# Kernel tuning notes

Hardware: AMD Instinct MI355X
Metric: run time of the kernel (lower is better)

The kernel has to match this reference:

```python
import jax, jax.numpy as jnp
import numpy as np

E = 8      # num_traits / experts
D = 1024   # input_size per trait
H = 2048   # hidden width (hidden_sizes = [2048, 2048] -> one hidden Linear)
O = 1024   # output_size
B = 4096   # batch
TOP_K = 2


def setup_inputs() -> dict:
    key = jax.random.key(0)
    ks = jax.random.split(key, E + 8)
    s = 0.02
    inp = {f"x{i}": jax.random.normal(ks[i], (B, D), dtype=jnp.float32) for i in range(E)}
    inp["gate_w"] = jax.random.normal(ks[E + 0], (E * D, E), dtype=jnp.float32) * s
    inp["gate_b"] = jnp.zeros((E,), dtype=jnp.float32)
    inp["w_in"]  = jax.random.normal(ks[E + 1], (E, D, H), dtype=jnp.float32) * s
    inp["b_in"]  = jnp.zeros((E, H), dtype=jnp.float32)
    inp["w_h"]   = jax.random.normal(ks[E + 2], (E, H, H), dtype=jnp.float32) * s
    inp["b_h"]   = jnp.zeros((E, H), dtype=jnp.float32)
    inp["w_out"] = jax.random.normal(ks[E + 3], (E, H, O), dtype=jnp.float32) * s
    inp["b_out"] = jnp.zeros((E, O), dtype=jnp.float32)
    return inp


def reference(x0, x1, x2, x3, x4, x5, x6, x7,
              gate_w, gate_b, w_in, b_in, w_h, b_h, w_out, b_out):
    xs_list = [x0, x1, x2, x3, x4, x5, x6, x7]
    xs = jnp.stack(xs_list, axis=0)                       # [E, B, D]
    combined = jnp.concatenate(xs_list, axis=1)           # [B, E*D]

    # gating: top-2 + softmax over selected logits, scattered to dense [B, E]
    gate_logits = combined @ gate_w + gate_b              # [B, E]
    topk_vals, topk_idx = jax.lax.top_k(gate_logits, TOP_K)
    topk_w = jax.nn.softmax(topk_vals, axis=1)
    bsz = gate_logits.shape[0]
    rows = jnp.arange(bsz)[:, None]
    dense_w = jnp.zeros_like(gate_logits).at[rows, topk_idx].set(topk_w)  # [B, E]

    # per-expert MLP (dropout inactive at inference; use_skip=False).
    # Computed densely for all tokens; unselected tokens get weight 0 in the
    # combine, matching the masked dispatch/scatter math exactly.
    h = jax.nn.relu(jnp.einsum('ebd,edh->ebh', xs, w_in) + b_in[:, None, :])   # [E, B, H]
    h = jax.nn.relu(jnp.einsum('ebh,ehk->ebk', h, w_h) + b_h[:, None, :])      # [E, B, H]
    expert_out = jnp.einsum('ebk,eko->ebo', h, w_out) + b_out[:, None, :]      # [E, B, O]

    # weighted combine: sum_e dense_w[b,e] * expert_out[e,b,:]
    moe_output = jnp.einsum('ebo,be->bo', expert_out, dense_w)                 # [B, O]
    return moe_output
```

## Files before the change

kernel.cpp:

```cpp
#include <hip/hip_runtime.h>
#include <stdint.h>

#define E_ 8
#define D_ 1024
#define H_ 2048
#define O_ 1024
#define B_ 4096
#define GTOT (B_ * 2)
#define GPAD (GTOT + 256)
#define MT_MAX 16
#define MT256 8

typedef __attribute__((ext_vector_type(8))) __bf16 bf16x8;
typedef __attribute__((ext_vector_type(4))) float f32x4;
typedef unsigned short u16;
typedef __attribute__((ext_vector_type(4))) u16 u16x4;
typedef __attribute__((ext_vector_type(8))) u16 u16x8;

__device__ __forceinline__ u16 f2bf(float f) {
    union { float f; uint32_t u; } v; v.f = f;
    uint32_t u = v.u;
    return (u16)((u + 0x7FFFu + ((u >> 16) & 1u)) >> 16);
}

__device__ __forceinline__ void gl2lds16(const void* g, void* lds) {
    __builtin_amdgcn_global_load_lds(
        (__attribute__((address_space(1))) void*)(uintptr_t)g,
        (__attribute__((address_space(3))) void*)(uint32_t)(uintptr_t)lds,
        16, 0, 0);
}

struct XPtrs { const float* p[8]; };

__device__ __forceinline__ void gate_finish(int b, const double* acc, const float* __restrict__ gb,
                                            int* __restrict__ t2i, float* __restrict__ t2w) {
    float lg[8];
#pragma unroll
    for (int e = 0; e < 8; ++e) lg[e] = (float)acc[e] + gb[e];
    int i0 = 0;
#pragma unroll
    for (int e = 1; e < 8; ++e) if (lg[e] > lg[i0]) i0 = e;
    int i1 = -1;
#pragma unroll
    for (int e = 0; e < 8; ++e) {
        if (e == i0) continue;
        if (i1 < 0 || lg[e] > lg[i1]) i1 = e;
    }
    float ex = expf(lg[i1] - lg[i0]);
    float w0 = 1.0f / (1.0f + ex);
    t2i[b * 2 + 0] = i0; t2i[b * 2 + 1] = i1;
    t2w[b * 2 + 0] = w0; t2w[b * 2 + 1] = ex * w0;
}

__global__ void __launch_bounds__(256) gate_kernel(XPtrs xs, const float* __restrict__ gw,
                                                   const float* __restrict__ gb,
                                                   int* __restrict__ t2i, float* __restrict__ t2w) {
    int wave = threadIdx.x >> 6;
    int lane = threadIdx.x & 63;
    int b0 = blockIdx.x * 8 + wave * 2;
    double acc0[8], acc1[8];
#pragma unroll
    for (int e = 0; e < 8; ++e) { acc0[e] = 0.0; acc1[e] = 0.0; }
    for (int ep = 0; ep < 8; ++ep) {
        const float* xr0 = xs.p[ep] + (size_t)b0 * D_;
        const float* xr1 = xr0 + D_;
        for (int t = 0; t < D_ / 64; ++t) {
            int d = t * 64 + lane;
            float v0 = xr0[d];
            float v1 = xr1[d];
            const float* g = gw + ((size_t)(ep * D_ + d)) * 8;
#pragma unroll
            for (int e = 0; e < 8; ++e) {
                double ge = (double)g[e];
                acc0[e] += (double)v0 * ge;
                acc1[e] += (double)v1 * ge;
            }
        }
    }
#pragma unroll
    for (int e = 0; e < 8; ++e) {
        for (int off = 32; off > 0; off >>= 1) {
            acc0[e] += __shfl_xor(acc0[e], off, 64);
            acc1[e] += __shfl_xor(acc1[e], off, 64);
        }
    }
    if (lane == 0) {
        gate_finish(b0 + 0, acc0, gb, t2i, t2w);
        gate_finish(b0 + 1, acc1, gb, t2i, t2w);
    }
}

__global__ void __launch_bounds__(256) route_build(const int* __restrict__ t2i,
                                                   int* __restrict__ offs, int* __restrict__ cursor) {
    __shared__ int cnt[8];
    int t = threadIdx.x;
    if (t < 8) cnt[t] = 0;
    __syncthreads();
    for (int i = t; i < B_ * 2; i += 256) atomicAdd(&cnt[t2i[i]], 1);
    __syncthreads();
    if (t == 0) {
        int run = 0;
        for (int e = 0; e < 8; ++e) { offs[e] = run; cursor[e] = run; run += cnt[e]; }
        offs[8] = run;
    }
}

__global__ void __launch_bounds__(256) scatter_gather(XPtrs xs, const int* __restrict__ t2i,
                                                      int* __restrict__ cursor, int* __restrict__ slot,
                                                      u16* __restrict__ A1) {
    int b = blockIdx.x;
    int t = threadIdx.x;
    __shared__ int gsh[2];
    int e0 = t2i[b * 2 + 0], e1 = t2i[b * 2 + 1];
    if (t == 0) {
        int g0 = atomicAdd(&cursor[e0], 1);
        int g1 = atomicAdd(&cursor[e1], 1);
        gsh[0] = g0; gsh[1] = g1;
        slot[b * 2 + 0] = g0; slot[b * 2 + 1] = g1;
    }
    __syncthreads();
    int g0 = gsh[0], g1 = gsh[1];
    float4 v0 = ((const float4*)(xs.p[e0] + (size_t)b * D_))[t];
    float4 v1 = ((const float4*)(xs.p[e1] + (size_t)b * D_))[t];
    u16x4 o0, o1;
    o0.x = f2bf(v0.x); o0.y = f2bf(v0.y); o0.z = f2bf(v0.z); o0.w = f2bf(v0.w);
    o1.x = f2bf(v1.x); o1.y = f2bf(v1.y); o1.z = f2bf(v1.z); o1.w = f2bf(v1.w);
    ((u16x4*)(A1 + (size_t)g0 * D_))[t] = o0;
    ((u16x4*)(A1 + (size_t)g1 * D_))[t] = o1;
}

__global__ void __launch_bounds__(256) wconv(const float* __restrict__ w, u16* __restrict__ wt,
                                             int K, int N) {
    __shared__ float tile[64][33];
    int e = blockIdx.z;
    int n0 = blockIdx.x * 32, k0 = blockIdx.y * 64;
    int tid = threadIdx.x;
    int tx = tid & 31, ty = tid >> 5;
    const float* wp = w + (size_t)e * K * N + (size_t)k0 * N + n0;
#pragma unroll
    for (int r = 0; r < 8; ++r)
        tile[ty + r * 8][tx] = wp[(size_t)(ty + r * 8) * N + tx];
    __syncthreads();
    int n = tid >> 3, kq = tid & 7;
    u16x8 o;
#pragma unroll
    for (int i = 0; i < 8; ++i) o[i] = f2bf(tile[kq * 8 + i][n]);
    u16* op = wt + (size_t)e * N * K + (size_t)(n0 + n) * K + k0 + kq * 8;
    *(u16x8*)op = o;
}

__global__ void __launch_bounds__(512, 2) expert_gemm256(const u16* __restrict__ A,
                                                         const u16* __restrict__ Wt,
                                                         const float* __restrict__ bias,
                                                         u16* __restrict__ outB,
                                                         const int* __restrict__ offs,
                                                         int K, int N) {
    int bid = blockIdx.x;
    int e = bid & 7;
    int j = bid >> 3;
    int mt = j & (MT256 - 1);
    int nt = j >> 3;
    int row0 = offs[e];
    int cnt = offs[e + 1] - row0;
    if (mt * 256 >= cnt) return;

    extern __shared__ __align__(16) u16 smem[];
    u16* sA = smem;
    u16* sB = smem + 32768;

    int tid = threadIdx.x;
    int wave = tid >> 6, lane = tid & 63;
    int wm = wave >> 2;
    int wn = wave & 3;
    int l15 = lane & 15, quad = lane >> 4;
    int swz = l15 & 7;

    const u16* Abase = A + (size_t)(row0 + mt * 256) * K;
    const u16* Bbase = Wt + ((size_t)e * N + (size_t)nt * 256) * K;
    int NT = K >> 6;

    auto stageA = [&](int tile, int half) {
        if (tile < NT) {
            u16* dst = sA + (((tile & 1) * 2 + half) << 13);
            const u16* gs = Abase + (size_t)(half * 128) * K + tile * 64;
#pragma unroll
            for (int rr = 0; rr < 2; ++rr) {
                int liB = rr * 512 + wave * 64;
                int li = liB + lane;
                int r = li >> 3;
                int lc = (li & 7) ^ (r & 7);
                gl2lds16(gs + (size_t)r * K + lc * 8, dst + liB * 8);
            }
        }
    };
    auto stageB = [&](int tile, int half) {
        if (tile < NT) {
            u16* dst = sB + (((tile & 1) * 2 + half) << 13);
            const u16* gs = Bbase + (size_t)(half * 128) * K + tile * 64;
#pragma unroll
            for (int rr = 0; rr < 2; ++rr) {
                int liB = rr * 512 + wave * 64;
                int li = liB + lane;
                int r = li >> 3;
                int lc = (li & 7) ^ (r & 7);
                gl2lds16(gs + (size_t)r * K + lc * 8, dst + liB * 8);
            }
        }
    };

    f32x4 acc[2][2][4][2];
#pragma unroll
    for (int a = 0; a < 2; ++a)
#pragma unroll
        for (int b = 0; b < 2; ++b)
#pragma unroll
            for (int c = 0; c < 4; ++c)
#pragma unroll
                for (int dd = 0; dd < 2; ++dd) acc[a][b][c][dd] = (f32x4){0.f, 0.f, 0.f, 0.f};

    stageA(0, 0); stageB(0, 0); stageA(0, 1); stageB(0, 1);
    stageA(1, 0); stageB(1, 0);
    __builtin_amdgcn_s_waitcnt(0x74);
    __builtin_amdgcn_s_barrier();

    bf16x8 af[4][2];
    bf16x8 bfr[2][2][2];

    for (int T = 0; T < NT; ++T) {
        int d = T & 1;
        const u16* aB0 = sA + ((d * 2 + 0) << 13);
        const u16* aB1 = sA + ((d * 2 + 1) << 13);
        const u16* bB0 = sB + ((d * 2 + 0) << 13);
        const u16* bB1 = sB + ((d * 2 + 1) << 13);

#pragma unroll
        for (int fm = 0; fm < 4; ++fm) {
            int rh = wm * 64 + fm * 16 + l15;
#pragma unroll
            for (int kc = 0; kc < 2; ++kc)
                af[fm][kc] = *(const bf16x8*)(aB0 + rh * 64 + (((kc << 2) | quad) ^ swz) * 8);
        }
#pragma unroll
        for (int fn = 0; fn < 2; ++fn) {
            int rh = wn * 32 + fn * 16 + l15;
#pragma unroll
            for (int kc = 0; kc < 2; ++kc)
                bfr[0][fn][kc] = *(const bf16x8*)(bB0 + rh * 64 + (((kc << 2) | quad) ^ swz) * 8);
        }
        stageA(T + 1, 1);
        __builtin_amdgcn_s_barrier();
        __builtin_amdgcn_s_setprio(1);
#pragma unroll
        for (int fm = 0; fm < 4; ++fm)
#pragma unroll
            for (int fn = 0; fn < 2; ++fn)
#pragma unroll
                for (int kc = 0; kc < 2; ++kc)
                    acc[0][0][fm][fn] = __builtin_amdgcn_mfma_f32_16x16x32_bf16(
                        af[fm][kc], bfr[0][fn][kc], acc[0][0][fm][fn], 0, 0, 0);
        __builtin_amdgcn_s_setprio(0);
        __builtin_amdgcn_s_barrier();

#pragma unroll
        for (int fn = 0; fn < 2; ++fn) {
            int rh = wn * 32 + fn * 16 + l15;
#pragma unroll
            for (int kc = 0; kc < 2; ++kc)
                bfr[1][fn][kc] = *(const bf16x8*)(bB1 + rh * 64 + (((kc << 2) | quad) ^ swz) * 8);
        }
        stageB(T + 1, 1);
        __builtin_amdgcn_s_barrier();
        __builtin_amdgcn_s_setprio(1);
#pragma unroll
        for (int fm = 0; fm < 4; ++fm)
#pragma unroll
            for (int fn = 0; fn < 2; ++fn)
#pragma unroll
                for (int kc = 0; kc < 2; ++kc)
                    acc[0][1][fm][fn] = __builtin_amdgcn_mfma_f32_16x16x32_bf16(
                        af[fm][kc], bfr[1][fn][kc], acc[0][1][fm][fn], 0, 0, 0);
        __builtin_amdgcn_s_setprio(0);
        __builtin_amdgcn_s_barrier();

#pragma unroll
        for (int fm = 0; fm < 4; ++fm) {
            int rh = wm * 64 + fm * 16 + l15;
#pragma unroll
            for (int kc = 0; kc < 2; ++kc)
                af[fm][kc] = *(const bf16x8*)(aB1 + rh * 64 + (((kc << 2) | quad) ^ swz) * 8);
        }
        stageA(T + 2, 0);
        __builtin_amdgcn_s_barrier();
        __builtin_amdgcn_s_setprio(1);
#pragma unroll
        for (int fm = 0; fm < 4; ++fm)
#pragma unroll
            for (int fn = 0; fn < 2; ++fn)
#pragma unroll
                for (int kc = 0; kc < 2; ++kc)
                    acc[1][0][fm][fn] = __builtin_amdgcn_mfma_f32_16x16x32_bf16(
                        af[fm][kc], bfr[0][fn][kc], acc[1][0][fm][fn], 0, 0, 0);
        __builtin_amdgcn_s_setprio(0);
        __builtin_amdgcn_s_barrier();

        stageB(T + 2, 0);
        __builtin_amdgcn_s_barrier();
        __builtin_amdgcn_s_setprio(1);
#pragma unroll
        for (int fm = 0; fm < 4; ++fm)
#pragma unroll
            for (int fn = 0; fn < 2; ++fn)
#pragma unroll
                for (int kc = 0; kc < 2; ++kc)
                    acc[1][1][fm][fn] = __builtin_amdgcn_mfma_f32_16x16x32_bf16(
                        af[fm][kc], bfr[1][fn][kc], acc[1][1][fm][fn], 0, 0, 0);
        __builtin_amdgcn_s_setprio(0);
        if (T + 2 < NT) __builtin_amdgcn_s_waitcnt(0x74);
        else            __builtin_amdgcn_s_waitcnt(0x70);
        __builtin_amdgcn_s_barrier();
    }

#pragma unroll
    for (int mh = 0; mh < 2; ++mh)
#pragma unroll
        for (int nh = 0; nh < 2; ++nh)
#pragma unroll
            for (int fn = 0; fn < 2; ++fn) {
                int col = nt * 256 + nh * 128 + wn * 32 + fn * 16 + l15;
                float bv = bias[e * N + col];
#pragma unroll
                for (int fm = 0; fm < 4; ++fm) {
                    int rloc = mt * 256 + mh * 128 + wm * 64 + fm * 16 + quad * 4;
#pragma unroll
                    for (int r = 0; r < 4; ++r) {
                        if (rloc + r < cnt) {
                            float v = acc[mh][nh][fm][fn][r] + bv;
                            v = fmaxf(v, 0.f);
                            outB[(size_t)(row0 + rloc + r) * N + col] = f2bf(v);
                        }
                    }
                }
            }
}

__global__ void __launch_bounds__(256) expert_gemm(const u16* __restrict__ A, const u16* __restrict__ Wt,
                                                   const float* __restrict__ bias,
                                                   u16* __restrict__ outB, float* __restrict__ outF,
                                                   const int* __restrict__ offs, int K, int N, int relu) {
    int bid = blockIdx.x;
    int e = bid & 7;
    int j = bid >> 3;
    int mt = j & (MT_MAX - 1);
    int nt = j >> 4;
    int row0 = offs[e];
    int cnt = offs[e + 1] - row0;
    if (mt * 128 >= cnt) return;

    __shared__ __align__(16) u16 sA[3][128 * 32];
    __shared__ __align__(16) u16 sB[3][128 * 32];

    int tid = threadIdx.x;
    int wave = tid >> 6, lane = tid & 63;
    int wm = wave & 1, wn = wave >> 1;
    int l15 = lane & 15, quad = lane >> 4;
    int rsub = lane >> 2;
    int koff = (((lane & 3) ^ (rsub & 3) ^ ((rsub >> 2) & 3)) * 8);
    int physOff = (quad ^ (l15 & 3) ^ ((l15 >> 2) & 3)) * 8;

    f32x4 acc[4][4];
#pragma unroll
    for (int i = 0; i < 4; ++i)
#pragma unroll
        for (int jj = 0; jj < 4; ++jj) acc[i][jj] = (f32x4){0.f, 0.f, 0.f, 0.f};

    const u16* Abase = A + (size_t)(row0 + mt * 128) * K;
    const u16* Bbase = Wt + ((size_t)e * N + (size_t)nt * 128) * K;

    int kSteps = K / 32;

    auto issue = [&](int ks, int bufIdx) {
        int k0 = ks * 32;
        u16* dA = &sA[bufIdx][0];
        u16* dB = &sB[bufIdx][0];
#pragma unroll
        for (int c = 0; c < 2; ++c) {
            int ch = wave * 2 + c;
            int r = ch * 16 + rsub;
            gl2lds16(Abase + (size_t)r * K + k0 + koff, dA + ch * 512);
            gl2lds16(Bbase + (size_t)r * K + k0 + koff, dB + ch * 512);
        }
    };

    issue(0, 0);
    issue(1, 1);
    int bc = 0, bi = 2;
    for (int ks = 0; ks < kSteps; ++ks) {
        if (ks + 1 < kSteps) __builtin_amdgcn_s_waitcnt(0x74);
        else                 __builtin_amdgcn_s_waitcnt(0x70);
        __builtin_amdgcn_s_barrier();
        if (ks + 2 < kSteps) issue(ks + 2, bi);

        const u16* a_ = &sA[bc][0];
        const u16* b_ = &sB[bc][0];
        bf16x8 af[4], bfr[4];
#pragma unroll
        for (int tm = 0; tm < 4; ++tm) {
            int row = wm * 64 + tm * 16 + l15;
            af[tm] = *(const bf16x8*)(a_ + row * 32 + physOff);
        }
#pragma unroll
        for (int tn = 0; tn < 4; ++tn) {
            int row = wn * 64 + tn * 16 + l15;
            bfr[tn] = *(const bf16x8*)(b_ + row * 32 + physOff);
        }
        __builtin_amdgcn_s_setprio(1);
#pragma unroll
        for (int tm = 0; tm < 4; ++tm)
#pragma unroll
            for (int tn = 0; tn < 4; ++tn)
                acc[tm][tn] = __builtin_amdgcn_mfma_f32_16x16x32_bf16(af[tm], bfr[tn], acc[tm][tn], 0, 0, 0);
        __builtin_amdgcn_s_setprio(0);

        bc = (bc == 2) ? 0 : bc + 1;
        bi = (bi == 2) ? 0 : bi + 1;
    }

    size_t gm0 = (size_t)row0 + (size_t)mt * 128 + (size_t)wm * 64;
    int lm0 = mt * 128 + wm * 64;
    int n0 = nt * 128 + wn * 64;
#pragma unroll
    for (int tn = 0; tn < 4; ++tn) {
        int col = n0 + tn * 16 + l15;
        float bv = bias[e * N + col];
#pragma unroll
        for (int tm = 0; tm < 4; ++tm) {
#pragma unroll
            for (int r = 0; r < 4; ++r) {
                int rr = tm * 16 + quad * 4 + r;
                if (lm0 + rr < cnt) {
                    float v = acc[tm][tn][r] + bv;
                    if (relu) v = fmaxf(v, 0.f);
                    if (outB) outB[(gm0 + rr) * N + col] = f2bf(v);
                    else      outF[(gm0 + rr) * N + col] = v;
                }
            }
        }
    }
}

__global__ void __launch_bounds__(256) combine_out(const float* __restrict__ eo, const int* __restrict__ slot,
                                                   const float* __restrict__ t2w, float* __restrict__ out) {
    int b = blockIdx.x, t = threadIdx.x;
    int g0 = slot[b * 2 + 0], g1 = slot[b * 2 + 1];
    float w0 = t2w[b * 2 + 0], w1 = t2w[b * 2 + 1];
    float4 va = ((const float4*)(eo + (size_t)g0 * O_))[t];
    float4 vc = ((const float4*)(eo + (size_t)g1 * O_))[t];
    float4 r;
    r.x = w0 * va.x + w1 * vc.x;
    r.y = w0 * va.y + w1 * vc.y;
    r.z = w0 * va.z + w1 * vc.z;
    r.w = w0 * va.w + w1 * vc.w;
    ((float4*)(out + (size_t)b * O_))[t] = r;
}

extern "C" void kernel_launch(void* const* d_in, const int* in_sizes, int n_in,
                              void* d_out, int out_size, void* d_ws, size_t ws_size,
                              hipStream_t stream) {
    (void)in_sizes; (void)n_in; (void)out_size; (void)ws_size;

    static bool lds_attr_set = false;
    if (!lds_attr_set) {
        hipFuncSetAttribute((const void*)expert_gemm256,
                            hipFuncAttributeMaxDynamicSharedMemorySize, 131072);
        lds_attr_set = true;
    }

    XPtrs xp;
    for (int i = 0; i < 8; ++i) xp.p[i] = (const float*)d_in[i];
    const float* gate_w = (const float*)d_in[8];
    const float* gate_b = (const float*)d_in[9];
    const float* w_in  = (const float*)d_in[10];
    const float* b_in  = (const float*)d_in[11];
    const float* w_h   = (const float*)d_in[12];
    const float* b_h   = (const float*)d_in[13];
    const float* w_out = (const float*)d_in[14];
    const float* b_out = (const float*)d_in[15];
    float* out = (float*)d_out;

    char* ws = (char*)d_ws;
    size_t off = 0;
    auto alloc = [&](size_t b) { size_t o = off; off += (b + 255) & ~(size_t)255; return o; };

    size_t t2i_o  = alloc((size_t)B_ * 2 * 4);
    size_t t2w_o  = alloc((size_t)B_ * 2 * 4);
    size_t slot_o = alloc((size_t)B_ * 2 * 4);
    size_t offs_o = alloc(16 * 4);
    size_t cur_o  = alloc(8 * 4);
    size_t A1_o   = alloc((size_t)GPAD * D_ * 2);
    size_t h1_o   = alloc((size_t)GPAD * H_ * 2);
    size_t h2_o   = alloc((size_t)GPAD * H_ * 2);
    size_t wtin_o = alloc((size_t)E_ * H_ * D_ * 2);
    size_t wth_o  = alloc((size_t)E_ * H_ * H_ * 2);
    size_t wtout_o= alloc((size_t)E_ * O_ * H_ * 2);
    size_t eo_o   = A1_o;

    int*   t2i  = (int*)(ws + t2i_o);
    float* t2w  = (float*)(ws + t2w_o);
    int*   slot = (int*)(ws + slot_o);
    int*   offs = (int*)(ws + offs_o);
    int*   cur  = (int*)(ws + cur_o);
    u16*   A1   = (u16*)(ws + A1_o);
    u16*   h1   = (u16*)(ws + h1_o);
    u16*   h2   = (u16*)(ws + h2_o);
    u16*   wtin = (u16*)(ws + wtin_o);
    u16*   wth  = (u16*)(ws + wth_o);
    u16*   wtout= (u16*)(ws + wtout_o);
    float* eo   = (float*)(ws + eo_o);

    hipLaunchKernelGGL(gate_kernel, dim3(B_ / 8), dim3(256), 0, stream, xp, gate_w, gate_b, t2i, t2w);
    hipLaunchKernelGGL(route_build, dim3(1), dim3(256), 0, stream, t2i, offs, cur);
    hipLaunchKernelGGL(scatter_gather, dim3(B_), dim3(256), 0, stream, xp, t2i, cur, slot, A1);

    hipLaunchKernelGGL(wconv, dim3(H_ / 32, D_ / 64, E_), dim3(256), 0, stream, w_in, wtin, D_, H_);
    hipLaunchKernelGGL(wconv, dim3(H_ / 32, H_ / 64, E_), dim3(256), 0, stream, w_h, wth, H_, H_);
    hipLaunchKernelGGL(wconv, dim3(O_ / 32, H_ / 64, E_), dim3(256), 0, stream, w_out, wtout, H_, O_);

    hipLaunchKernelGGL(expert_gemm256, dim3(E_ * MT256 * (H_ / 256)), dim3(512), 131072, stream,
                       A1, wtin, b_in, h1, offs, D_, H_);
    hipLaunchKernelGGL(expert_gemm256, dim3(E_ * MT256 * (H_ / 256)), dim3(512), 131072, stream,
                       h1, wth, b_h, h2, offs, H_, H_);
    hipLaunchKernelGGL(expert_gemm, dim3(E_ * MT_MAX * (O_ / 128)), dim3(256), 0, stream,
                       h2, wtout, b_out, (u16*)nullptr, eo, offs, H_, O_, 0);

    hipLaunchKernelGGL(combine_out, dim3(B_), dim3(256), 0, stream, eo, slot, t2w, out);
}
```

Before: 838.9 us.

## Double-buffer LDS fragment registers to overlap reads with MFMA in GEMM loop

Reorganizes the main GEMM k-loop so LDS-to-register fragment reads for the next quadrant (and next tile) are issued before the current MFMA block runs. It uses separate A and B register buffers and adjusts the waitcnt values to match. The goal is to hide LDS read latency behind matrix instructions and remove stalls at quadrant boundaries. In exchange it raises VGPR pressure, which could hurt occupancy, and it depends on finely tuned waitcnt encodings being correct.

```diff
diff --git a/kernel.cpp b/kernel.cpp
--- a/kernel.cpp
+++ b/kernel.cpp
@@ -208,6 +208,40 @@
         }
     };
 
+    bf16x8 afA[4][2], afB[4][2];
+    bf16x8 bf0[2][2], bf1[2][2];
+
+    auto readA = [&](bf16x8 (&dst)[4][2], const u16* base) {
+#pragma unroll
+        for (int fm = 0; fm < 4; ++fm) {
+            int rh = wm * 64 + fm * 16 + l15;
+#pragma unroll
+            for (int kc = 0; kc < 2; ++kc)
+                dst[fm][kc] = *(const bf16x8*)(base + rh * 64 + (((kc << 2) | quad) ^ swz) * 8);
+        }
+    };
+    auto readB = [&](bf16x8 (&dst)[2][2], const u16* base) {
+#pragma unroll
+        for (int fn = 0; fn < 2; ++fn) {
+            int rh = wn * 32 + fn * 16 + l15;
+#pragma unroll
+            for (int kc = 0; kc < 2; ++kc)
+                dst[fn][kc] = *(const bf16x8*)(base + rh * 64 + (((kc << 2) | quad) ^ swz) * 8);
+        }
+    };
+    auto mfmaQ = [&](bf16x8 (&a)[4][2], bf16x8 (&b)[2][2], f32x4 (&ac)[4][2]) {
+        __builtin_amdgcn_s_setprio(1);
+#pragma unroll
+        for (int fm = 0; fm < 4; ++fm)
+#pragma unroll
+            for (int fn = 0; fn < 2; ++fn)
+#pragma unroll
+                for (int kc = 0; kc < 2; ++kc)
+                    ac[fm][fn] = __builtin_amdgcn_mfma_f32_16x16x32_bf16(
+                        a[fm][kc], b[fn][kc], ac[fm][fn], 0, 0, 0);
+        __builtin_amdgcn_s_setprio(0);
+    };
+
     f32x4 acc[2][2][4][2];
 #pragma unroll
     for (int a = 0; a < 2; ++a)
@@ -220,105 +254,52 @@
 
     stageA(0, 0); stageB(0, 0); stageA(0, 1); stageB(0, 1);
     stageA(1, 0); stageB(1, 0);
-    __builtin_amdgcn_s_waitcnt(0x74);
+    __builtin_amdgcn_s_waitcnt(0x78);
     __builtin_amdgcn_s_barrier();
-
-    bf16x8 af[4][2];
-    bf16x8 bfr[2][2][2];
+    readA(afA, sA);
+    readB(bf0, sB);
+    __builtin_amdgcn_s_waitcnt(0xF74);
+    __builtin_amdgcn_s_barrier();
 
     for (int T = 0; T < NT; ++T) {
-        int d = T & 1;
-        const u16* aB0 = sA + ((d * 2 + 0) << 13);
-        const u16* aB1 = sA + ((d * 2 + 1) << 13);
-        const u16* bB0 = sB + ((d * 2 + 0) << 13);
-        const u16* bB1 = sB + ((d * 2 + 1) << 13);
-
-#pragma unroll
-        for (int fm = 0; fm < 4; ++fm) {
-            int rh = wm * 64 + fm * 16 + l15;
-#pragma unroll
-            for (int kc = 0; kc < 2; ++kc)
-                af[fm][kc] = *(const bf16x8*)(aB0 + rh * 64 + (((kc << 2) | quad) ^ swz) * 8);
-        }
-#pragma unroll
-        for (int fn = 0; fn < 2; ++fn) {
-            int rh = wn * 32 + fn * 16 + l15;
-#pragma unroll
-            for (int kc = 0; kc < 2; ++kc)
-                bfr[0][fn][kc] = *(const bf16x8*)(bB0 + rh * 64 + (((kc << 2) | quad) ^ swz) * 8);
-        }
+        int d = T & 1, dn = d ^ 1;
+        const u16* aB1p = sA + ((d * 2 + 1) << 13);
+        const u16* bB1p = sB + ((d * 2 + 1) << 13);
+        const u16* aB0n = sA + ((dn * 2 + 0) << 13);
+        const u16* bB0n = sB + ((dn * 2 + 0) << 13);
+        int steady = (T + 2 < NT);
+
+        readB(bf1, bB1p);
         stageA(T + 1, 1);
         __builtin_amdgcn_s_barrier();
-        __builtin_amdgcn_s_setprio(1);
-#pragma unroll
-        for (int fm = 0; fm < 4; ++fm)
-#pragma unroll
-            for (int fn = 0; fn < 2; ++fn)
-#pragma unroll
-                for (int kc = 0; kc < 2; ++kc)
-                    acc[0][0][fm][fn] = __builtin_amdgcn_mfma_f32_16x16x32_bf16(
-                        af[fm][kc], bfr[0][fn][kc], acc[0][0][fm][fn], 0, 0, 0);
-        __builtin_amdgcn_s_setprio(0);
-        __builtin_amdgcn_s_barrier();
-
-#pragma unroll
-        for (int fn = 0; fn < 2; ++fn) {
-            int rh = wn * 32 + fn * 16 + l15;
-#pragma unroll
-            for (int kc = 0; kc < 2; ++kc)
-                bfr[1][fn][kc] = *(const bf16x8*)(bB1 + rh * 64 + (((kc << 2) | quad) ^ swz) * 8);
-        }
+        mfmaQ(afA, bf0, acc[0][0]);
+        __builtin_amdgcn_s_barrier();
+
+        readA(afB, aB1p);
         stageB(T + 1, 1);
         __builtin_amdgcn_s_barrier();
-        __builtin_amdgcn_s_setprio(1);
-#pragma unroll
-        for (int fm = 0; fm < 4; ++fm)
-#pragma unroll
-            for (int fn = 0; fn < 2; ++fn)
-#pragma unroll
-                for (int kc = 0; kc < 2; ++kc)
-                    acc[0][1][fm][fn] = __builtin_amdgcn_mfma_f32_16x16x32_bf16(
-                        af[fm][kc], bfr[1][fn][kc], acc[0][1][fm][fn], 0, 0, 0);
-        __builtin_amdgcn_s_setprio(0);
-        __builtin_amdgcn_s_barrier();
-
-#pragma unroll
-        for (int fm = 0; fm < 4; ++fm) {
-            int rh = wm * 64 + fm * 16 + l15;
-#pragma unroll
-            for (int kc = 0; kc < 2; ++kc)
-                af[fm][kc] = *(const bf16x8*)(aB1 + rh * 64 + (((kc << 2) | quad) ^ swz) * 8);
-        }
+        mfmaQ(afA, bf1, acc[0][1]);
+        __builtin_amdgcn_s_barrier();
+
         stageA(T + 2, 0);
         __builtin_amdgcn_s_barrier();
-        __builtin_amdgcn_s_setprio(1);
-#pragma unroll
-        for (int fm = 0; fm < 4; ++fm)
-#pragma unroll
-            for (int fn = 0; fn < 2; ++fn)
-#pragma unroll
-                for (int kc = 0; kc < 2; ++kc)
-                    acc[1][0][fm][fn] = __builtin_amdgcn_mfma_f32_16x16x32_bf16(
-                        af[fm][kc], bfr[0][fn][kc], acc[1][0][fm][fn], 0, 0, 0);
-        __builtin_amdgcn_s_setprio(0);
+        mfmaQ(afB, bf0, acc[1][0]);
         __builtin_amdgcn_s_barrier();
 
         stageB(T + 2, 0);
-        __builtin_amdgcn_s_barrier();
-        __builtin_amdgcn_s_setprio(1);
-#pragma unroll
-        for (int fm = 0; fm < 4; ++fm)
-#pragma unroll
-            for (int fn = 0; fn < 2; ++fn)
-#pragma unroll
-                for (int kc = 0; kc < 2; ++kc)
-                    acc[1][1][fm][fn] = __builtin_amdgcn_mfma_f32_16x16x32_bf16(
-                        af[fm][kc], bfr[1][fn][kc], acc[1][1][fm][fn], 0, 0, 0);
-        __builtin_amdgcn_s_setprio(0);
-        if (T + 2 < NT) __builtin_amdgcn_s_waitcnt(0x74);
-        else            __builtin_amdgcn_s_waitcnt(0x70);
-        __builtin_amdgcn_s_barrier();
-    }
+        if (steady) __builtin_amdgcn_s_waitcnt(0x78);
+        else        __builtin_amdgcn_s_waitcnt(0x70);
+        __builtin_amdgcn_s_barrier();
+        if (T + 1 < NT) {
+            readA(afA, aB0n);
+            readB(bf0, bB0n);
+        }
+        mfmaQ(afB, bf1, acc[1][1]);
+        if (steady) __builtin_amdgcn_s_waitcnt(0xF74);
+        else        __builtin_amdgcn_s_waitcnt(0xF70);
+        __builtin_amdgcn_s_barrier();
+    }
+    __builtin_amdgcn_s_waitcnt(0x70);
 
 #pragma unroll
     for (int mh = 0; mh < 2; ++mh)
```

After: 827.6 us. Within noise of the previous version (-1.4%).
